# Kernel optimization log

Hardware: AMD Instinct MI355X
Metric: run time of the kernel (lower is better)

The kernel has to match this reference:

```python
import jax, jax.numpy as jnp
import numpy as np

TARGET_RADIUS = 0.99

def setup_inputs() -> dict:
    key = jax.random.key(0)
    k1, k2, k3 = jax.random.split(key, 3)
    T, B, D = 2048, 16, 1024
    x = jax.random.normal(k1, (T, B, D), dtype=jnp.float32)
    h0 = jnp.zeros((B, D), dtype=jnp.float32)
    # xavier_uniform for W_x: bound = sqrt(6/(D+D))
    bound = float(np.sqrt(6.0 / (D + D)))
    W_x = jax.random.uniform(k2, (D, D), dtype=jnp.float32, minval=-bound, maxval=bound)
    # d init: uniform(0.9, 0.99)
    d = jax.random.uniform(k3, (D,), dtype=jnp.float32, minval=0.9, maxval=0.99)
    b = jnp.zeros((D,), dtype=jnp.float32)
    return {"x": x, "h0": h0, "W_x": W_x, "d": d, "b": b}

def reference(x, h0, W_x, d, b):
    # Spectral constraint on diagonal recurrence
    d_c = jnp.clip(d, -TARGET_RADIUS, TARGET_RADIUS)
    # Batch the per-timestep input GEMM into one big matmul: [T,B,D] @ [D,D]^T
    xw = jnp.einsum('tbd,ed->tbe', x, W_x) + b  # [T, B, D]

    def step(h_prev, xw_t):
        h_new = jnp.tanh(xw_t + d_c * h_prev)      # [B, D]
        out_t = h_new * jax.nn.silu(h_new)          # self-gating
        return h_new, (h_new, out_t)

    _, (hs, output) = jax.lax.scan(step, h0, xw)
    h = jnp.concatenate([h0[None], hs], axis=0)     # [T+1, B, D]
    return output, h
```

## Files before the change

### kernel.cpp

```cpp
#include <hip/hip_runtime.h>

#define TT 2048
#define BB 16
#define DD 1024
#define BD (BB * DD)

typedef _Float16 f16;
typedef _Float16 f16x8 __attribute__((ext_vector_type(8)));
typedef float f32x4 __attribute__((ext_vector_type(4)));
typedef float f32x2 __attribute__((ext_vector_type(2)));
typedef unsigned int u32;

__device__ __forceinline__ void gload_lds16(const void* g, const void* s) {
    const __attribute__((address_space(1))) u32* gp =
        (const __attribute__((address_space(1))) u32*)(unsigned long long)(size_t)g;
    __attribute__((address_space(3))) u32* sp =
        (__attribute__((address_space(3))) u32*)(u32)(size_t)s;
    __builtin_amdgcn_global_load_lds(gp, sp, 16, 0, 0);
}

__global__ __launch_bounds__(256) void cvt_f16(const float* __restrict__ in,
                                               f16* __restrict__ out, int n8) {
    int i = blockIdx.x * 256 + threadIdx.x;
    const int stride = gridDim.x * 256;
    for (; i < n8; i += stride) {
        const float4* p = (const float4*)in + (size_t)i * 2;
        float4 a = p[0], b = p[1];
        f16x8 o;
        o[0] = (f16)a.x; o[1] = (f16)a.y; o[2] = (f16)a.z; o[3] = (f16)a.w;
        o[4] = (f16)b.x; o[5] = (f16)b.y; o[6] = (f16)b.z; o[7] = (f16)b.w;
        *((f16x8*)out + i) = o;
    }
}

__global__ __launch_bounds__(256) void gemm_f16(const f16* __restrict__ A,
                                                const f16* __restrict__ W,
                                                float* __restrict__ C) {
    __shared__ f16 As[128 * 64];
    __shared__ f16 Bs[128 * 64];

    const int tid = threadIdx.x;

    const int flat = blockIdx.y * gridDim.x + blockIdx.x;
    const int xcd = flat & 7;
    const int j = flat >> 3;
    const int rows_per_xcd = gridDim.y >> 3;
    const int bm = (xcd * rows_per_xcd + (j >> 3)) * 128;
    const int bn = (j & 7) * 128;

    const int sm = tid >> 3;
    const int ss = tid & 7;
    const int kb = ss ^ (sm & 7);

    const f16* Ag = A + (size_t)(bm + sm) * DD + kb * 8;
    const f16* Bg = W + (size_t)(bn + sm) * DD + kb * 8;

    const int wave = tid >> 6;
    const int lane = tid & 63;
    const int wm = (wave & 1) * 64;
    const int wn = (wave >> 1) * 64;
    const int fr = lane & 15;
    const int quad = lane >> 4;

    f32x4 acc[4][4];
#pragma unroll
    for (int i = 0; i < 4; ++i)
#pragma unroll
        for (int j2 = 0; j2 < 4; ++j2) acc[i][j2] = (f32x4){0.f, 0.f, 0.f, 0.f};

    for (int kt = 0; kt < 16; ++kt) {
        const f16* Agk = Ag + kt * 64;
        const f16* Bgk = Bg + kt * 64;
        __syncthreads();
#pragma unroll
        for (int r = 0; r < 4; ++r) {
            gload_lds16(Agk + (size_t)r * 32 * DD, (const char*)As + (r * 256 + tid) * 16);
            gload_lds16(Bgk + (size_t)r * 32 * DD, (const char*)Bs + (r * 256 + tid) * 16);
        }
        __syncthreads();

#pragma unroll
        for (int ks = 0; ks < 2; ++ks) {
            f16x8 af[4], bf[4];
#pragma unroll
            for (int i = 0; i < 4; ++i) {
                const int row = wm + i * 16 + fr;
                const int slot = (ks * 4 + quad) ^ (row & 7);
                af[i] = *(const f16x8*)((const char*)As + row * 128 + slot * 16);
            }
#pragma unroll
            for (int j2 = 0; j2 < 4; ++j2) {
                const int row = wn + j2 * 16 + fr;
                const int slot = (ks * 4 + quad) ^ (row & 7);
                bf[j2] = *(const f16x8*)((const char*)Bs + row * 128 + slot * 16);
            }
#pragma unroll
            for (int i = 0; i < 4; ++i)
#pragma unroll
                for (int j2 = 0; j2 < 4; ++j2)
                    acc[i][j2] = __builtin_amdgcn_mfma_f32_16x16x32_f16(af[i], bf[j2], acc[i][j2], 0, 0, 0);
        }
    }

#pragma unroll
    for (int i = 0; i < 4; ++i) {
        const int gm = bm + wm + i * 16 + quad * 4;
#pragma unroll
        for (int j2 = 0; j2 < 4; ++j2) {
            const int gn = bn + wn + j2 * 16 + fr;
            float* cp = C + (size_t)gm * DD + gn;
#pragma unroll
            for (int r = 0; r < 4; ++r)
                cp[(size_t)r * DD] = acc[i][j2][r];
        }
    }
}

__device__ __forceinline__ void cell2(f32x2 v, f32x2 d2, f32x2& h, f32x2& o) {
#pragma unroll
    for (int c = 0; c < 2; ++c) {
        const float z = fmaf(d2[c], h[c], v[c]);
        const float E = __expf(z);
        const float t = fmaf(-2.f, __builtin_amdgcn_rcpf(E + 1.f), 1.f);
        h[c] = t;
        const float s = __builtin_amdgcn_rcpf(1.f + __expf(-t));
        o[c] = t * t * s;
    }
}

__global__ __launch_bounds__(64) void scan_step(const float* __restrict__ xw,
                                                const float* __restrict__ dvec,
                                                const float* __restrict__ bvec,
                                                const float* __restrict__ h0,
                                                float* __restrict__ out,
                                                float* __restrict__ hout,
                                                int Tc, int first) {
    const int p = blockIdx.x * 64 + threadIdx.x;
    const int l = p * 2;
    const int e = l & (DD - 1);

    const f32x2 dv = *(const f32x2*)(dvec + e);
    const f32x2 bv = *(const f32x2*)(bvec + e);
    f32x2 d2, b2;
    d2.x = 2.f * fminf(fmaxf(dv.x, -0.99f), 0.99f);
    d2.y = 2.f * fminf(fmaxf(dv.y, -0.99f), 0.99f);
    b2.x = 2.f * bv.x;
    b2.y = 2.f * bv.y;

    f32x2 h;
    if (first) {
        h = *(const f32x2*)(h0 + l);
        *(f32x2*)(hout + l) = h;
    } else {
        h = *(const f32x2*)(hout + l);
    }

    const float* xp = xw + l;
    f32x2 va[16], vb[16];
#pragma unroll
    for (int i = 0; i < 16; ++i) {
        f32x2 x = *(const f32x2*)(xp + (size_t)i * BD);
        va[i] = x + x + b2;
    }

    for (int t0 = 0; t0 < Tc; t0 += 32) {
#pragma unroll
        for (int i = 0; i < 16; ++i) {
            f32x2 x = *(const f32x2*)(xp + (size_t)(t0 + 16 + i) * BD);
            vb[i] = x + x + b2;
        }
#pragma unroll
        for (int i = 0; i < 16; ++i) {
            f32x2 o;
            cell2(va[i], d2, h, o);
            __builtin_nontemporal_store(o, (f32x2*)(out + (size_t)(t0 + i) * BD + l));
            __builtin_nontemporal_store(h, (f32x2*)(hout + (size_t)(t0 + i + 1) * BD + l));
        }
        if (t0 + 32 < Tc) {
#pragma unroll
            for (int i = 0; i < 16; ++i) {
                f32x2 x = *(const f32x2*)(xp + (size_t)(t0 + 32 + i) * BD);
                va[i] = x + x + b2;
            }
        }
#pragma unroll
        for (int i = 0; i < 16; ++i) {
            f32x2 o;
            cell2(vb[i], d2, h, o);
            __builtin_nontemporal_store(o, (f32x2*)(out + (size_t)(t0 + 16 + i) * BD + l));
            __builtin_nontemporal_store(h, (f32x2*)(hout + (size_t)(t0 + 16 + i + 1) * BD + l));
        }
    }
}

extern "C" void kernel_launch(void* const* d_in, const int* in_sizes, int n_in,
                              void* d_out, int out_size, void* d_ws, size_t ws_size,
                              hipStream_t stream) {
    const float* x  = (const float*)d_in[0];
    const float* h0 = (const float*)d_in[1];
    const float* Wx = (const float*)d_in[2];
    const float* dv = (const float*)d_in[3];
    const float* bv = (const float*)d_in[4];

    float* out  = (float*)d_out;
    float* hout = out + (size_t)TT * BD;

    f16* Wf = (f16*)d_ws;
    const size_t wbytes = (size_t)DD * DD * sizeof(f16);
    const size_t rem = (ws_size > wbytes) ? ws_size - wbytes : 0;
    long long Tc = (long long)(rem / ((size_t)BD * 6));
    Tc = (Tc / 64) * 64;
    if (Tc > TT) Tc = TT;
    if (Tc < 64) Tc = 64;

    f16*   xf = (f16*)((char*)d_ws + wbytes);
    float* xw = (float*)((char*)d_ws + wbytes + (size_t)Tc * BD * 2);

    cvt_f16<<<512, 256, 0, stream>>>(Wx, Wf, DD * DD / 8);

    for (int t0 = 0; t0 < TT; ) {
        int tc = (int)Tc;
        if (tc > TT - t0) tc = TT - t0;
        const int n8 = tc * BD / 8;
        cvt_f16<<<2048, 256, 0, stream>>>(x + (size_t)t0 * BD, xf, n8);
        dim3 grid(DD / 128, tc * BB / 128);
        gemm_f16<<<grid, 256, 0, stream>>>(xf, Wf, xw);
        scan_step<<<BD / 128, 64, 0, stream>>>(xw, dv, bv, h0,
                                               out  + (size_t)t0 * BD,
                                               hout + (size_t)t0 * BD,
                                               tc, t0 == 0);
        t0 += tc;
    }
}
```

Before: 601.6 us.

## Split scan into compute and store waves with LDS double buffer

The scan kernel is restructured into 128-thread blocks. One wave runs the serial recurrence on one channel per lane with four-deep slab prefetch of xw, and writes outputs and hidden states into double-buffered LDS. A second wave drains LDS to global memory with nontemporal stores, taking the store traffic off the critical recurrence path. The sigmoid is also replaced with a polynomial in tanh, and the block count doubles to 256. The polynomial adds approximation error, and the per-slab barriers couple the two waves.

```diff
diff --git a/kernel.cpp b/kernel.cpp
--- a/kernel.cpp
+++ b/kernel.cpp
@@ -4,11 +4,11 @@
 #define BB 16
 #define DD 1024
 #define BD (BB * DD)
+#define SLAB 16
 
 typedef _Float16 f16;
 typedef _Float16 f16x8 __attribute__((ext_vector_type(8)));
 typedef float f32x4 __attribute__((ext_vector_type(4)));
-typedef float f32x2 __attribute__((ext_vector_type(2)));
 typedef unsigned int u32;
 
 __device__ __forceinline__ void gload_lds16(const void* g, const void* s) {
@@ -116,79 +116,89 @@
     }
 }
 
-__device__ __forceinline__ void cell2(f32x2 v, f32x2 d2, f32x2& h, f32x2& o) {
-#pragma unroll
-    for (int c = 0; c < 2; ++c) {
-        const float z = fmaf(d2[c], h[c], v[c]);
-        const float E = __expf(z);
-        const float t = fmaf(-2.f, __builtin_amdgcn_rcpf(E + 1.f), 1.f);
-        h[c] = t;
-        const float s = __builtin_amdgcn_rcpf(1.f + __expf(-t));
-        o[c] = t * t * s;
-    }
-}
-
-__global__ __launch_bounds__(64) void scan_step(const float* __restrict__ xw,
-                                                const float* __restrict__ dvec,
-                                                const float* __restrict__ bvec,
-                                                const float* __restrict__ h0,
-                                                float* __restrict__ out,
-                                                float* __restrict__ hout,
-                                                int Tc, int first) {
-    const int p = blockIdx.x * 64 + threadIdx.x;
-    const int l = p * 2;
-    const int e = l & (DD - 1);
-
-    const f32x2 dv = *(const f32x2*)(dvec + e);
-    const f32x2 bv = *(const f32x2*)(bvec + e);
-    f32x2 d2, b2;
-    d2.x = 2.f * fminf(fmaxf(dv.x, -0.99f), 0.99f);
-    d2.y = 2.f * fminf(fmaxf(dv.y, -0.99f), 0.99f);
-    b2.x = 2.f * bv.x;
-    b2.y = 2.f * bv.y;
-
-    f32x2 h;
-    if (first) {
-        h = *(const f32x2*)(h0 + l);
-        *(f32x2*)(hout + l) = h;
+__global__ __launch_bounds__(128) void scan_step(const float* __restrict__ xw,
+                                                 const float* __restrict__ dvec,
+                                                 const float* __restrict__ bvec,
+                                                 const float* __restrict__ h0,
+                                                 float* __restrict__ out,
+                                                 float* __restrict__ hout,
+                                                 int Tc, int first) {
+    __shared__ float o_lds[2][SLAB][64];
+    __shared__ float h_lds[2][SLAB][64];
+
+    const int lane = threadIdx.x & 63;
+    const int wid  = threadIdx.x >> 6;
+    const int c0   = blockIdx.x * 64;
+    const int l    = c0 + lane;
+    const int S    = Tc / SLAB;
+
+    if (wid == 0) {
+        const int e = l & (DD - 1);
+        const float dc = fminf(fmaxf(dvec[e], -0.99f), 0.99f);
+        const float d2 = 2.f * dc;
+        const float b2 = 2.f * bvec[e];
+
+        float h = first ? h0[l] : hout[l];
+
+        const float* xp = xw + l;
+        float A[SLAB], B[SLAB], C[SLAB], D[SLAB];
+
+#define LOADSLAB(buf, s_) do {                                          \
+        const float* _p = xp + (size_t)(s_) * SLAB * BD;                \
+        _Pragma("unroll")                                               \
+        for (int _i = 0; _i < SLAB; ++_i) buf[_i] = _p[(size_t)_i * BD]; \
+    } while (0)
+
+#define COMPUTE(buf, par) do {                                          \
+        _Pragma("unroll")                                               \
+        for (int _i = 0; _i < SLAB; ++_i) {                             \
+            const float v2 = fmaf(2.f, buf[_i], b2);                    \
+            const float z  = fmaf(d2, h, v2);                   \
+            const float E  = __expf(z);                                 \
+            const float t  = fmaf(-2.f, __builtin_amdgcn_rcpf(E + 1.f), 1.f); \
+            h = t;                                                      \
+            const float t2 = t * t;                                     \
+            const float pp = fmaf(t2, fmaf(t2, fmaf(t2, -2.108134e-4f,  \
+                                2.0833334e-3f), -2.0833334e-2f), 0.25f);\
+            const float sg = fmaf(t, pp, 0.5f);         \
+            o_lds[par][_i][lane] = t2 * sg;                             \
+            h_lds[par][_i][lane] = t;                                   \
+        }                                                               \
+    } while (0)
+
+        LOADSLAB(A, 0); LOADSLAB(B, 1); LOADSLAB(C, 2);
+        for (int s = 0; s < S; s += 4) {
+            if (s + 3 < S) LOADSLAB(D, s + 3);
+            COMPUTE(A, 0);
+            __syncthreads();
+            if (s + 4 < S) LOADSLAB(A, s + 4);
+            COMPUTE(B, 1);
+            __syncthreads();
+            if (s + 5 < S) LOADSLAB(B, s + 5);
+            COMPUTE(C, 0);
+            __syncthreads();
+            if (s + 6 < S) LOADSLAB(C, s + 6);
+            COMPUTE(D, 1);
+            __syncthreads();
+        }
+#undef LOADSLAB
+#undef COMPUTE
     } else {
-        h = *(const f32x2*)(hout + l);
-    }
-
-    const float* xp = xw + l;
-    f32x2 va[16], vb[16];
-#pragma unroll
-    for (int i = 0; i < 16; ++i) {
-        f32x2 x = *(const f32x2*)(xp + (size_t)i * BD);
-        va[i] = x + x + b2;
-    }
-
-    for (int t0 = 0; t0 < Tc; t0 += 32) {
-#pragma unroll
-        for (int i = 0; i < 16; ++i) {
-            f32x2 x = *(const f32x2*)(xp + (size_t)(t0 + 16 + i) * BD);
-            vb[i] = x + x + b2;
-        }
-#pragma unroll
-        for (int i = 0; i < 16; ++i) {
-            f32x2 o;
-            cell2(va[i], d2, h, o);
-            __builtin_nontemporal_store(o, (f32x2*)(out + (size_t)(t0 + i) * BD + l));
-            __builtin_nontemporal_store(h, (f32x2*)(hout + (size_t)(t0 + i + 1) * BD + l));
-        }
-        if (t0 + 32 < Tc) {
-#pragma unroll
-            for (int i = 0; i < 16; ++i) {
-                f32x2 x = *(const f32x2*)(xp + (size_t)(t0 + 32 + i) * BD);
-                va[i] = x + x + b2;
+        if (first) {
+            __builtin_nontemporal_store(h0[l], hout + l);
+        }
+        for (int s = 0; s < S; ++s) {
+            __syncthreads();
+            const int par = s & 1;
+            float* po = out  + (size_t)(s * SLAB) * BD + l;
+            float* ph = hout + (size_t)(s * SLAB + 1) * BD + l;
+#pragma unroll
+            for (int t = 0; t < SLAB; ++t) {
+                const float ov = o_lds[par][t][lane];
+                const float hv = h_lds[par][t][lane];
+                __builtin_nontemporal_store(ov, po + (size_t)t * BD);
+                __builtin_nontemporal_store(hv, ph + (size_t)t * BD);
             }
-        }
-#pragma unroll
-        for (int i = 0; i < 16; ++i) {
-            f32x2 o;
-            cell2(vb[i], d2, h, o);
-            __builtin_nontemporal_store(o, (f32x2*)(out + (size_t)(t0 + 16 + i) * BD + l));
-            __builtin_nontemporal_store(h, (f32x2*)(hout + (size_t)(t0 + 16 + i + 1) * BD + l));
         }
     }
 }
@@ -225,7 +235,7 @@
         cvt_f16<<<2048, 256, 0, stream>>>(x + (size_t)t0 * BD, xf, n8);
         dim3 grid(DD / 128, tc * BB / 128);
         gemm_f16<<<grid, 256, 0, stream>>>(xf, Wf, xw);
-        scan_step<<<BD / 128, 64, 0, stream>>>(xw, dv, bv, h0,
+        scan_step<<<BD / 64, 128, 0, stream>>>(xw, dv, bv, h0,
                                                out  + (size_t)t0 * BD,
                                                hout + (size_t)t0 * BD,
                                                tc, t0 == 0);
```

New measurement: 514.0 us. -14.6%, faster.
